# Kernel tuning notes

Hardware: AMD Instinct MI355X
Metric: run time of the kernel (lower is better)

Reference implementation:

```python
import jax, jax.numpy as jnp
import numpy as np

N_STREAMS = 8
SINKHORN_ITER = 20
KERNEL_SIZE = 5
BANDWIDTH = 0.5
PAD = KERNEL_SIZE // 2
EPS = 1e-8


def _gaussian_kernel():
    x = jnp.arange(KERNEL_SIZE, dtype=jnp.float32) - KERNEL_SIZE // 2
    xx, yy = jnp.meshgrid(x, x, indexing='ij')
    k = jnp.exp(-(xx ** 2 + yy ** 2) / (2.0 * BANDWIDTH ** 2))
    k = k / k.sum()
    return k.reshape(1, 1, KERNEL_SIZE, KERNEL_SIZE)  # OIHW


def setup_inputs() -> dict:
    key = jax.random.key(0)
    B, H, W = 32, 128, 128
    log_H_res = jax.random.normal(key, (B, N_STREAMS * N_STREAMS, H, W), dtype=jnp.float32)
    return {"log_H_res": log_H_res, "gaussian_kernel": _gaussian_kernel()}


def reference(log_H_res, gaussian_kernel):
    B, C, H, W = log_H_res.shape
    n = N_STREAMS
    H_lin = jnp.exp(log_H_res.reshape(B, n, n, H, W))

    def smooth(m):
        # m: (B, n, H, W) linear-domain marginal; circular pad + 5x5 Gaussian conv
        x = m.reshape(B * n, 1, H, W)
        x = jnp.pad(x, ((0, 0), (0, 0), (PAD, PAD), (PAD, PAD)), mode='wrap')
        y = jax.lax.conv_general_dilated(
            x, gaussian_kernel, window_strides=(1, 1), padding='VALID',
            dimension_numbers=('NCHW', 'OIHW', 'NCHW'))
        return y.reshape(B, n, H, W)

    def body(_, Hl):
        row = smooth(Hl.sum(axis=2))[:, :, None]   # (B, n, 1, H, W)
        Hl = Hl / (row + EPS)
        col = smooth(Hl.sum(axis=1))[:, None]      # (B, 1, n, H, W)
        Hl = Hl / (col + EPS)
        return Hl

    H_lin = jax.lax.fori_loop(0, SINKHORN_ITER, body, H_lin)
    # faithful to original: log then exp with eps stabilization
    H_star = jnp.exp(jnp.log(H_lin + EPS))
    return H_star  # (B, n, n, H, W)
```

## Files before the change

### kernel.cpp

```cpp
#include <hip/hip_runtime.h>

#define NS    8
#define HGT   128
#define WID   128
#define HW    (HGT * WID)
#define BATCH 32
#define EPSV  1e-8f
#define ITERS 20

#define TH   8
#define LH   (TH + 4)
#define LW   132

typedef float4 f4;
typedef float2 f2;
typedef _Float16 half4 __attribute__((ext_vector_type(4)));
typedef _Float16 half2v __attribute__((ext_vector_type(2)));

__global__ __launch_bounds__(256) void k_init(const float* __restrict__ logH,
                                              _Float16* __restrict__ H0h,
                                              float* __restrict__ mrow) {
    int gid = blockIdx.x * 256 + threadIdx.x;
    int e = gid * 4;
    int p = e & (HW - 1);
    int c = (e >> 14) & 7;
    int b = e >> 17;
    int base = ((b * NS + c) * NS) * HW + p;
    f4 s = {0.f, 0.f, 0.f, 0.f};
#pragma unroll
    for (int j = 0; j < NS; ++j) {
        f4 l = *(const f4*)(logH + base + j * HW);
        f4 ev;
        ev.x = __expf(l.x); ev.y = __expf(l.y);
        ev.z = __expf(l.z); ev.w = __expf(l.w);
        half4 h;
        h.x = (_Float16)ev.x; h.y = (_Float16)ev.y;
        h.z = (_Float16)ev.z; h.w = (_Float16)ev.w;
        *(half4*)(H0h + base + j * HW) = h;
        s.x += ev.x; s.y += ev.y; s.z += ev.z; s.w += ev.w;
    }
    *(f4*)(mrow + e) = s;
}

__device__ __forceinline__ void stage_tile(const float* __restrict__ m_in,
                                           int b, int ty0, int tid,
                                           float tile[NS][LH][LW]) {
#pragma unroll
    for (int c = 0; c < NS; ++c) {
        const float* src = m_in + (b * NS + c) * HW;
        if (tid < LH * 32) {
            int ly = tid >> 5, lxq = tid & 31;
            int gh = (ty0 + ly - 2 + HGT) & (HGT - 1);
            f4 val = *(const f4*)(src + gh * WID + lxq * 4);
            float* dst = &tile[c][ly][2 + lxq * 4];
            dst[0] = val.x; dst[1] = val.y; dst[2] = val.z; dst[3] = val.w;
        } else if (tid >= 512 - LH * 4) {
            int t = tid - (512 - LH * 4);
            int ly = t >> 2, e = t & 3;
            int gh = (ty0 + ly - 2 + HGT) & (HGT - 1);
            int x  = (e < 2) ? (126 + e) : (e - 2);
            int hx = (e < 2) ? e : (128 + e);
            tile[c][ly][hx] = src[gh * WID + x];
        }
    }
}

__device__ __forceinline__ f2 conv5(const float (*tc)[LW], const float* wk,
                                    int ly, int lx2) {
    float s0 = 0.f, s1 = 0.f;
#pragma unroll
    for (int dy = 0; dy < 5; ++dy) {
        const float* row = &tc[ly + dy][lx2 * 2];
        f2 A = *(const f2*)row;
        f2 B = *(const f2*)(row + 2);
        f2 C = *(const f2*)(row + 4);
        float vv[6] = {A.x, A.y, B.x, B.y, C.x, C.y};
#pragma unroll
        for (int dx = 0; dx < 5; ++dx) {
            float w = wk[dy * 5 + dx];
            s0 += w * vv[dx];
            s1 += w * vv[dx + 1];
        }
    }
    return f2{s0, s1};
}

template <int ROWSTEP, int FIRST>
__global__ __launch_bounds__(512, 4) void k_step(const float* __restrict__ m_in,
                                                 float* __restrict__ a,
                                                 const float* __restrict__ bvec,
                                                 float* __restrict__ m_out,
                                                 const _Float16* __restrict__ H0h,
                                                 const float* __restrict__ gk) {
    __shared__ float tile[NS][LH][LW];
    __shared__ float wk[25];
    int tid = threadIdx.x;
    int b   = blockIdx.z;
    int ty0 = blockIdx.y * TH;
    if (tid < 25) wk[tid] = gk[tid];

    stage_tile(m_in, b, ty0, tid, tile);
    __syncthreads();

    int lx2 = tid & 63;
    int ly  = tid >> 6;
    int p   = (ty0 + ly) * WID + lx2 * 2;

    f2 av[NS];
#pragma unroll
    for (int c = 0; c < NS; ++c) {
        f2 s = conv5(tile[c], wk, ly, lx2);
        int ai = (b * NS + c) * HW + p;
        f2 un;
        if (FIRST) {
            un.x = 1.f / (s.x + EPSV);
            un.y = 1.f / (s.y + EPSV);
        } else {
            f2 ao = *(const f2*)(a + ai);
            un.x = ao.x / (s.x + EPSV);
            un.y = ao.y / (s.y + EPSV);
        }
        *(f2*)(a + ai) = un;
        av[c] = un;
    }

    f2 acc[NS];
#pragma unroll
    for (int cp = 0; cp < NS; ++cp) acc[cp] = f2{0.f, 0.f};
    const _Float16* Hb = H0h + b * NS * NS * HW + p;
#pragma unroll
    for (int c = 0; c < NS; ++c) {
        f2 x = av[c];
#pragma unroll
        for (int cp = 0; cp < NS; ++cp) {
            int ch = ROWSTEP ? (c * NS + cp) : (cp * NS + c);
            half2v h = *(const half2v*)(Hb + ch * HW);
            acc[cp].x += (float)h.x * x.x;
            acc[cp].y += (float)h.y * x.y;
        }
    }
#pragma unroll
    for (int cp = 0; cp < NS; ++cp) {
        int oi = (b * NS + cp) * HW + p;
        f2 o;
        if (ROWSTEP && FIRST) {
            o = acc[cp];
        } else {
            f2 bv = *(const f2*)(bvec + oi);
            o.x = bv.x * acc[cp].x;
            o.y = bv.y * acc[cp].y;
        }
        *(f2*)(m_out + oi) = o;
    }
}

__global__ __launch_bounds__(512, 4) void k_last(const float* __restrict__ m_in,
                                                 const float* __restrict__ v,
                                                 const float* __restrict__ u,
                                                 const float* __restrict__ logH,
                                                 float* __restrict__ out,
                                                 const float* __restrict__ gk) {
    __shared__ float tile[NS][LH][LW];
    __shared__ float wk[25];
    int tid = threadIdx.x;
    int b   = blockIdx.z;
    int ty0 = blockIdx.y * TH;
    if (tid < 25) wk[tid] = gk[tid];

    stage_tile(m_in, b, ty0, tid, tile);
    __syncthreads();

    int lx2 = tid & 63;
    int ly  = tid >> 6;
    int p   = (ty0 + ly) * WID + lx2 * 2;

    f2 av[NS];
#pragma unroll
    for (int c = 0; c < NS; ++c) {
        f2 s = conv5(tile[c], wk, ly, lx2);
        f2 vo = *(const f2*)(v + (b * NS + c) * HW + p);
        av[c].x = vo.x / (s.x + EPSV);
        av[c].y = vo.y / (s.y + EPSV);
    }

    const float* Lb = logH + b * NS * NS * HW + p;
    float* Ob = out + b * NS * NS * HW + p;
#pragma unroll
    for (int i = 0; i < NS; ++i) {
        f2 uu = *(const f2*)(u + (b * NS + i) * HW + p);
#pragma unroll
        for (int j = 0; j < NS; ++j) {
            f2 l = *(const f2*)(Lb + (i * NS + j) * HW);
            f2 o;
            o.x = expf(l.x) * uu.x * av[j].x + EPSV;
            o.y = expf(l.y) * uu.y * av[j].y + EPSV;
            *(f2*)(Ob + (i * NS + j) * HW) = o;
        }
    }
}

extern "C" void kernel_launch(void* const* d_in, const int* in_sizes, int n_in,
                              void* d_out, int out_size, void* d_ws, size_t ws_size,
                              hipStream_t stream) {
    const float* logH = (const float*)d_in[0];
    const float* gk   = (const float*)d_in[1];
    float* out = (float*)d_out;
    _Float16* H0h = (_Float16*)d_out;
    float* ws = (float*)d_ws;
    const int VEC = BATCH * NS * HW;
    float* u    = ws;
    float* v    = ws + VEC;
    float* mrow = ws + 2 * (size_t)VEC;
    float* mcol = ws + 3 * (size_t)VEC;

    k_init<<<VEC / 4 / 256, 256, 0, stream>>>(logH, H0h, mrow);

    dim3 grid(1, HGT / TH, BATCH);
    k_step<1, 1><<<grid, 512, 0, stream>>>(mrow, u, v, mcol, H0h, gk);
    k_step<0, 1><<<grid, 512, 0, stream>>>(mcol, v, u, mrow, H0h, gk);
    for (int it = 1; it < ITERS; ++it) {
        k_step<1, 0><<<grid, 512, 0, stream>>>(mrow, u, v, mcol, H0h, gk);
        if (it != ITERS - 1) {
            k_step<0, 0><<<grid, 512, 0, stream>>>(mcol, v, u, mrow, H0h, gk);
        } else {
            k_last<<<grid, 512, 0, stream>>>(mcol, v, u, logH, out, gk);
        }
    }
}
```

Before: 1.361 ms.

## Store fp16 H matrix pixel-major for 16-byte vector loads

Changes the fp16 copy of exp(H) from channel-planar layout to a per-pixel 8x8 contiguous layout, so each thread reads whole rows of the 8x8 matrix with 16-byte loads instead of 64 scattered 4-byte loads. The column step reads the transpose from the same layout by indexing differently. k_init is rewritten to produce the new layout with one thread per pixel. The occupancy hint in launch_bounds is also raised from 4 to 6. Per-wave accesses are now strided by 128 bytes per pixel, which may hurt coalescing, and the higher occupancy target may force register spills.

```diff
diff --git a/kernel.cpp b/kernel.cpp
--- a/kernel.cpp
+++ b/kernel.cpp
@@ -14,32 +14,29 @@
 
 typedef float4 f4;
 typedef float2 f2;
-typedef _Float16 half4 __attribute__((ext_vector_type(4)));
-typedef _Float16 half2v __attribute__((ext_vector_type(2)));
+typedef _Float16 half8 __attribute__((ext_vector_type(8)));
 
 __global__ __launch_bounds__(256) void k_init(const float* __restrict__ logH,
                                               _Float16* __restrict__ H0h,
                                               float* __restrict__ mrow) {
     int gid = blockIdx.x * 256 + threadIdx.x;
-    int e = gid * 4;
-    int p = e & (HW - 1);
-    int c = (e >> 14) & 7;
-    int b = e >> 17;
-    int base = ((b * NS + c) * NS) * HW + p;
-    f4 s = {0.f, 0.f, 0.f, 0.f};
-#pragma unroll
-    for (int j = 0; j < NS; ++j) {
-        f4 l = *(const f4*)(logH + base + j * HW);
-        f4 ev;
-        ev.x = __expf(l.x); ev.y = __expf(l.y);
-        ev.z = __expf(l.z); ev.w = __expf(l.w);
-        half4 h;
-        h.x = (_Float16)ev.x; h.y = (_Float16)ev.y;
-        h.z = (_Float16)ev.z; h.w = (_Float16)ev.w;
-        *(half4*)(H0h + base + j * HW) = h;
-        s.x += ev.x; s.y += ev.y; s.z += ev.z; s.w += ev.w;
-    }
-    *(f4*)(mrow + e) = s;
+    int p = gid & (HW - 1);
+    int b = gid >> 14;
+    const float* Lb = logH + (size_t)(b * NS * NS) * HW + p;
+    _Float16* Hp = H0h + ((size_t)b * HW + p) * (NS * NS);
+#pragma unroll
+    for (int i = 0; i < NS; ++i) {
+        float s = 0.f;
+        half8 h;
+#pragma unroll
+        for (int j = 0; j < NS; ++j) {
+            float e = __expf(Lb[(i * NS + j) * HW]);
+            h[j] = (_Float16)e;
+            s += e;
+        }
+        *(half8*)(Hp + i * NS) = h;
+        mrow[(b * NS + i) * HW + p] = s;
+    }
 }
 
 __device__ __forceinline__ void stage_tile(const float* __restrict__ m_in,
@@ -86,7 +83,7 @@
 }
 
 template <int ROWSTEP, int FIRST>
-__global__ __launch_bounds__(512, 4) void k_step(const float* __restrict__ m_in,
+__global__ __launch_bounds__(512, 6) void k_step(const float* __restrict__ m_in,
                                                  float* __restrict__ a,
                                                  const float* __restrict__ bvec,
                                                  float* __restrict__ m_out,
@@ -127,16 +124,24 @@
     f2 acc[NS];
 #pragma unroll
     for (int cp = 0; cp < NS; ++cp) acc[cp] = f2{0.f, 0.f};
-    const _Float16* Hb = H0h + b * NS * NS * HW + p;
-#pragma unroll
-    for (int c = 0; c < NS; ++c) {
-        f2 x = av[c];
-#pragma unroll
-        for (int cp = 0; cp < NS; ++cp) {
-            int ch = ROWSTEP ? (c * NS + cp) : (cp * NS + c);
-            half2v h = *(const half2v*)(Hb + ch * HW);
-            acc[cp].x += (float)h.x * x.x;
-            acc[cp].y += (float)h.y * x.y;
+    const _Float16* Hp = H0h + ((size_t)b * HW + p) * (NS * NS);
+#pragma unroll
+    for (int c = 0; c < NS; ++c) {
+        half8 h0 = *(const half8*)(Hp + c * NS);
+        half8 h1 = *(const half8*)(Hp + NS * NS + c * NS);
+        if (ROWSTEP) {
+            f2 x = av[c];
+#pragma unroll
+            for (int cp = 0; cp < NS; ++cp) {
+                acc[cp].x += (float)h0[cp] * x.x;
+                acc[cp].y += (float)h1[cp] * x.y;
+            }
+        } else {
+#pragma unroll
+            for (int j = 0; j < NS; ++j) {
+                acc[c].x += (float)h0[j] * av[j].x;
+                acc[c].y += (float)h1[j] * av[j].y;
+            }
         }
     }
 #pragma unroll
@@ -154,7 +159,7 @@
     }
 }
 
-__global__ __launch_bounds__(512, 4) void k_last(const float* __restrict__ m_in,
+__global__ __launch_bounds__(512, 6) void k_last(const float* __restrict__ m_in,
                                                  const float* __restrict__ v,
                                                  const float* __restrict__ u,
                                                  const float* __restrict__ logH,
@@ -207,13 +212,13 @@
     float* out = (float*)d_out;
     _Float16* H0h = (_Float16*)d_out;
     float* ws = (float*)d_ws;
-    const int VEC = BATCH * NS * HW;
+    const size_t VEC = (size_t)BATCH * NS * HW;
     float* u    = ws;
     float* v    = ws + VEC;
-    float* mrow = ws + 2 * (size_t)VEC;
-    float* mcol = ws + 3 * (size_t)VEC;
-
-    k_init<<<VEC / 4 / 256, 256, 0, stream>>>(logH, H0h, mrow);
+    float* mrow = ws + 2 * VEC;
+    float* mcol = ws + 3 * VEC;
+
+    k_init<<<BATCH * HW / 256, 256, 0, stream>>>(logH, H0h, mrow);
 
     dim3 grid(1, HGT / TH, BATCH);
     k_step<1, 1><<<grid, 512, 0, stream>>>(mrow, u, v, mcol, H0h, gk);
```

Result: slower. 2.231 ms (+63.9%).
